# Performance work log

Measured on AMD Instinct MI355X. Metric: run time of the kernel, lower is better.

## Reference

```python
import jax, jax.numpy as jnp
import numpy as np

DIM = 768; HEADS = 12; HD = DIM // HEADS; SCALE = HD ** -0.5
B = 4; T = 8; H = 14; W = 14; N = H * W  # 196 VMAE patches per frame
DOWN = 192   # adapter down dim = dim * 0.25
MLP_H = 3072 # dim * mlp_ratio

def _ln(x, g, b, eps=1e-5):
    m = x.mean(-1, keepdims=True)
    v = ((x - m) ** 2).mean(-1, keepdims=True)
    return (x - m) * jax.lax.rsqrt(v + eps) * g + b

def _lin(x, w, b=None):
    y = x @ w.T
    return y if b is None else y + b

def _gelu(x):
    return jax.nn.gelu(x, approximate=False)  # torch nn.GELU (erf)

def _mha(q, k, v):  # q:[b,h,n,d] k,v:[b,h,m,d]
    a = jax.nn.softmax((q * SCALE) @ jnp.swapaxes(k, -2, -1), axis=-1)
    return a @ v

def _adapter(x, w1, b1, w2, b2, skip):
    y = _lin(_gelu(_lin(x, w1, b1)), w2, b2)
    return x + y if skip else y

def _block(s_x, t_x, p):
    # --- self-attention on temporal (VMAE) tokens, with adapter ---
    xn = _ln(t_x, p['g1'], p['bb1'])
    bias = jnp.concatenate([p['q_bias'], jnp.zeros_like(p['v_bias']), p['v_bias']])
    Bx, Nx, _ = xn.shape
    qkv = _lin(xn, p['qkv_w'], bias).reshape(Bx, Nx, 3, HEADS, HD).transpose(2, 0, 3, 1, 4)
    o = _mha(qkv[0], qkv[1], qkv[2]).transpose(0, 2, 1, 3).reshape(Bx, Nx, DIM)
    o = _lin(o, p['aproj_w'], p['aproj_b'])
    t = t_x + _adapter(o, p['sa_w1'], p['sa_b1'], p['sa_w2'], p['sa_b2'], True)
    # --- S2T cross-attn: temporal queries attend to per-frame CNN spatial tokens ---
    s_pat = s_x.reshape(B * T, H * W, DIM) + p['s2t_pos_cnn']
    tx = t.reshape(B * T, N, DIM) + p['s2t_pos_vmae']
    q = _lin(tx, p['s2t_qw'], p['s2t_qb']).reshape(B * T, N, HEADS, HD).transpose(0, 2, 1, 3)
    kv = _lin(s_pat, p['s2t_kvw'], p['s2t_kvb']).reshape(B * T, H * W, 2, HEADS, HD).transpose(2, 0, 3, 1, 4)
    o = _mha(q, kv[0], kv[1]).transpose(0, 2, 1, 3).reshape(B * T, N, DIM)
    o = _lin(o, p['s2t_pw'], p['s2t_pb']).reshape(B, T * N, DIM)
    t = t + o
    # --- T2S cross-attn: per-location CNN queries attend over time to VMAE tokens ---
    s_pat = s_x.reshape(B, T, H * W, DIM).transpose(0, 2, 1, 3) + p['t2s_pos_cnn']  # b hw t c
    tx = t.reshape(B, T, N, DIM).transpose(0, 2, 1, 3) + p['t2s_pos_vmae']          # b n t d (N==H*W)
    s_pat = s_pat.reshape(B * H * W, T, DIM)
    tx = tx.reshape(B * N, T, DIM)
    q = _lin(s_pat, p['t2s_qw'], p['t2s_qb']).reshape(B * H * W, T, HEADS, HD).transpose(0, 2, 1, 3)
    kv = _lin(tx, p['t2s_kvw'], p['t2s_kvb']).reshape(B * N, T, 2, HEADS, HD).transpose(2, 0, 3, 1, 4)
    o = _mha(q, kv[0], kv[1]).transpose(0, 2, 1, 3).reshape(B * H * W, T, DIM)
    o = _lin(o, p['t2s_pw'], p['t2s_pb'])
    s = s_x + o.reshape(B, H, W, T, DIM).transpose(0, 3, 1, 2, 4).reshape(B * T, H, W, DIM)
    # --- MLP + parallel adapter (scale = 0.5 per Block.__init__) ---
    xn2 = _ln(t, p['g2'], p['bb2'])
    t = t + _lin(_gelu(_lin(xn2, p['fc1_w'], p['fc1_b'])), p['fc2_w'], p['fc2_b']) \
          + 0.5 * _adapter(xn2, p['ma_w1'], p['ma_b1'], p['ma_w2'], p['ma_b2'], False)
    return s, t

PARAM_NAMES = ['g1','bb1','qkv_w','q_bias','v_bias','aproj_w','aproj_b',
               'sa_w1','sa_b1','sa_w2','sa_b2',
               's2t_pos_cnn','s2t_pos_vmae','s2t_qw','s2t_qb','s2t_kvw','s2t_kvb','s2t_pw','s2t_pb',
               't2s_pos_cnn','t2s_pos_vmae','t2s_qw','t2s_qb','t2s_kvw','t2s_kvb','t2s_pw','t2s_pb',
               'g2','bb2','fc1_w','fc1_b','fc2_w','fc2_b','ma_w1','ma_b1','ma_w2','ma_b2']

def setup_inputs():
    key = jax.random.key(0)
    ks = iter(jax.random.split(key, 64))
    def w(shape, s=0.02):
        return jax.random.normal(next(ks), shape, jnp.float32) * s
    d = dict(
        s_x=jax.random.normal(next(ks), (B * T, H, W, DIM), jnp.float32),
        t_x=jax.random.normal(next(ks), (B, T * N, DIM), jnp.float32),
        g1=jnp.ones((DIM,), jnp.float32), bb1=jnp.zeros((DIM,), jnp.float32),
        qkv_w=w((3 * DIM, DIM)), q_bias=jnp.zeros((DIM,), jnp.float32), v_bias=jnp.zeros((DIM,), jnp.float32),
        aproj_w=w((DIM, DIM)), aproj_b=jnp.zeros((DIM,), jnp.float32),
        sa_w1=w((DOWN, DIM)), sa_b1=jnp.zeros((DOWN,), jnp.float32),
        sa_w2=w((DIM, DOWN)), sa_b2=jnp.zeros((DIM,), jnp.float32),
        s2t_pos_cnn=w((H * W, DIM), SCALE), s2t_pos_vmae=w((196, DIM), SCALE),
        s2t_qw=w((DIM, DIM)), s2t_qb=jnp.zeros((DIM,), jnp.float32),
        s2t_kvw=w((2 * DIM, DIM)), s2t_kvb=jnp.zeros((2 * DIM,), jnp.float32),
        s2t_pw=w((DIM, DIM)), s2t_pb=jnp.zeros((DIM,), jnp.float32),
        t2s_pos_cnn=w((T, DIM), SCALE), t2s_pos_vmae=w((T, DIM), SCALE),
        t2s_qw=w((DIM, DIM)), t2s_qb=jnp.zeros((DIM,), jnp.float32),
        t2s_kvw=w((2 * DIM, DIM)), t2s_kvb=jnp.zeros((2 * DIM,), jnp.float32),
        t2s_pw=w((DIM, DIM)), t2s_pb=jnp.zeros((DIM,), jnp.float32),
        g2=jnp.ones((DIM,), jnp.float32), bb2=jnp.zeros((DIM,), jnp.float32),
        fc1_w=w((MLP_H, DIM)), fc1_b=jnp.zeros((MLP_H,), jnp.float32),
        fc2_w=w((DIM, MLP_H)), fc2_b=jnp.zeros((DIM,), jnp.float32),
        ma_w1=w((DOWN, DIM)), ma_b1=jnp.zeros((DOWN,), jnp.float32),
        ma_w2=w((DIM, DOWN)), ma_b2=jnp.zeros((DIM,), jnp.float32),
    )
    return d

def reference(s_x, t_x, g1, bb1, qkv_w, q_bias, v_bias, aproj_w, aproj_b,
              sa_w1, sa_b1, sa_w2, sa_b2,
              s2t_pos_cnn, s2t_pos_vmae, s2t_qw, s2t_qb, s2t_kvw, s2t_kvb, s2t_pw, s2t_pb,
              t2s_pos_cnn, t2s_pos_vmae, t2s_qw, t2s_qb, t2s_kvw, t2s_kvb, t2s_pw, t2s_pb,
              g2, bb2, fc1_w, fc1_b, fc2_w, fc2_b, ma_w1, ma_b1, ma_w2, ma_b2):
    loc = locals()
    p = {k: loc[k] for k in PARAM_NAMES}
    return _block(s_x, t_x, p)
```

## Files before the change

kernel.cpp:

```cpp
#include <hip/hip_runtime.h>
#include <hip/hip_bf16.h>
#include <math.h>


typedef __bf16 bf16_t;
typedef bf16_t bf16x4 __attribute__((ext_vector_type(4)));
typedef bf16_t bf16x8 __attribute__((ext_vector_type(8)));
typedef float  f32x4  __attribute__((ext_vector_type(4)));

typedef const __attribute__((address_space(1))) void* gas_t;
typedef __attribute__((address_space(3))) void* las_t;
__device__ __forceinline__ void async16(const void* g, void* l) {
    __builtin_amdgcn_global_load_lds((gas_t)g, (las_t)l, 16, 0, 0);
}

#define MFMA(a,b,c) __builtin_amdgcn_mfma_f32_16x16x32_bf16((a),(b),(c),0,0,0)
#define EXP2(x) __builtin_amdgcn_exp2f(x)
#define LOG2E 1.4426950408889634f

template<bool GELU>
__global__ __launch_bounds__(256) void gemm128(
    const bf16_t* __restrict__ A, const bf16_t* __restrict__ W,
    const float* __restrict__ bias,
    const float* __restrict__ res1, const float* __restrict__ res2,
    float res2_scale,
    float* __restrict__ Yf, bf16_t* __restrict__ Yb,
    int M, int N, int K)
{
    __shared__ bf16_t As[128*64];
    __shared__ bf16_t Bs[128*64];
    const int tid = threadIdx.x, wave = tid >> 6, lane = tid & 63;
    const int m0 = blockIdx.y * 128, n0 = blockIdx.x * 128;
    const int wm = (wave & 1) * 64, wn = (wave >> 1) * 64;
    const int l15 = lane & 15, lq = lane >> 4;
    const int lrow = lane >> 3, lcol = (lane & 7) * 8;

    f32x4 acc[4][4] = {};

    for (int k0 = 0; k0 < K; k0 += 64) {
#pragma unroll
        for (int c = 0; c < 4; ++c) {
            const int r = wave * 32 + c * 8;
            async16(A + (size_t)(m0 + r + lrow) * K + k0 + lcol, &As[r * 64]);
            async16(W + (size_t)(n0 + r + lrow) * K + k0 + lcol, &Bs[r * 64]);
        }
        __syncthreads();
#pragma unroll
        for (int kk = 0; kk < 64; kk += 32) {
            bf16x8 a[4], b[4];
#pragma unroll
            for (int i = 0; i < 4; ++i)
                a[i] = *(const bf16x8*)&As[(wm + i * 16 + l15) * 64 + kk + lq * 8];
#pragma unroll
            for (int i = 0; i < 4; ++i)
                b[i] = *(const bf16x8*)&Bs[(wn + i * 16 + l15) * 64 + kk + lq * 8];
#pragma unroll
            for (int mi = 0; mi < 4; ++mi)
#pragma unroll
                for (int ni = 0; ni < 4; ++ni)
                    acc[mi][ni] = MFMA(a[mi], b[ni], acc[mi][ni]);
        }
        __syncthreads();
    }

#pragma unroll
    for (int mi = 0; mi < 4; ++mi)
#pragma unroll
    for (int ni = 0; ni < 4; ++ni) {
        const int gn = n0 + wn + ni * 16 + l15;
        const float bv = bias ? bias[gn] : 0.f;
#pragma unroll
        for (int i = 0; i < 4; ++i) {
            const int gm = m0 + wm + mi * 16 + lq * 4 + i;
            float v = acc[mi][ni][i] + bv;
            if (GELU) v = 0.5f * v * (1.0f + erff(v * 0.70710678118654752f));
            const size_t off = (size_t)gm * N + gn;
            if (res1) v += res1[off];
            if (res2) v += res2_scale * res2[off];
            if (Yf) Yf[off] = v;
            if (Yb) Yb[off] = (bf16_t)v;
        }
    }
}

template<bool GELU, int EPI>
__global__ __launch_bounds__(256) void gemm128x64(
    const bf16_t* __restrict__ A, const bf16_t* __restrict__ W,
    const float* __restrict__ bias,
    const float* __restrict__ res1, const float* __restrict__ res2,
    float res2_scale,
    float* __restrict__ Yf, bf16_t* __restrict__ Yb,
    int M, int N, int K,
    const float* __restrict__ ep_a, float* __restrict__ ep_fo,
    bf16_t* __restrict__ ep_bo)
{
    __shared__ bf16_t As[128*64];
    __shared__ bf16_t Bs[64*64];
    const int tid = threadIdx.x, wave = tid >> 6, lane = tid & 63;
    const int m0 = blockIdx.y * 128, n0 = blockIdx.x * 64;
    const int wm = (wave & 1) * 64, wn = (wave >> 1) * 32;
    const int l15 = lane & 15, lq = lane >> 4;
    const int lrow = lane >> 3, lcol = (lane & 7) * 8;

    f32x4 acc[4][2] = {};

    for (int k0 = 0; k0 < K; k0 += 64) {
#pragma unroll
        for (int c = 0; c < 4; ++c) {
            const int r = wave * 32 + c * 8;
            async16(A + (size_t)(m0 + r + lrow) * K + k0 + lcol, &As[r * 64]);
        }
#pragma unroll
        for (int c = 0; c < 2; ++c) {
            const int r = wave * 16 + c * 8;
            async16(W + (size_t)(n0 + r + lrow) * K + k0 + lcol, &Bs[r * 64]);
        }
        __syncthreads();
#pragma unroll
        for (int kk = 0; kk < 64; kk += 32) {
            bf16x8 a[4], b[2];
#pragma unroll
            for (int i = 0; i < 4; ++i)
                a[i] = *(const bf16x8*)&As[(wm + i * 16 + l15) * 64 + kk + lq * 8];
#pragma unroll
            for (int i = 0; i < 2; ++i)
                b[i] = *(const bf16x8*)&Bs[(wn + i * 16 + l15) * 64 + kk + lq * 8];
#pragma unroll
            for (int mi = 0; mi < 4; ++mi)
#pragma unroll
                for (int ni = 0; ni < 2; ++ni)
                    acc[mi][ni] = MFMA(a[mi], b[ni], acc[mi][ni]);
        }
        __syncthreads();
    }

#pragma unroll
    for (int mi = 0; mi < 4; ++mi)
#pragma unroll
    for (int ni = 0; ni < 2; ++ni) {
        const int gn = n0 + wn + ni * 16 + l15;
        const float bv = bias ? bias[gn] : 0.f;
#pragma unroll
        for (int i = 0; i < 4; ++i) {
            const int gm = m0 + wm + mi * 16 + lq * 4 + i;
            float v = acc[mi][ni][i] + bv;
            if (GELU) v = 0.5f * v * (1.0f + erff(v * 0.70710678118654752f));
            const size_t off = (size_t)gm * N + gn;
            if (res1) v += res1[off];
            if (res2) v += res2_scale * res2[off];
            if (Yf) Yf[off] = v;
            if (Yb) Yb[off] = (bf16_t)v;
            if (EPI == 1) {
                const int b_ = gm / 1568, r_ = gm - b_ * 1568;
                const int t_ = r_ / 196,  n_ = r_ - t_ * 196;
                const int dest = ((b_ * 196 + n_) << 3) + t_;
                ep_bo[(size_t)dest * 768 + gn] =
                    (bf16_t)(v + ep_a[t_ * 768 + gn]);
            }
            if (EPI == 2) {
                const int t_ = gm & 7, bn_ = gm >> 3;
                const int n_ = bn_ % 196, b_ = bn_ / 196;
                const int dest = (b_ * 8 + t_) * 196 + n_;
                const size_t doff = (size_t)dest * 768 + gn;
                ep_fo[doff] = ep_a[doff] + v;
            }
        }
    }
}

template<bool GELU, int EPI>
__global__ __launch_bounds__(256) void gemm_bt(
    const float* __restrict__ X, const float* __restrict__ W,
    const float* __restrict__ bias,
    const float* __restrict__ res1, const float* __restrict__ res2,
    float res2_scale,
    float* __restrict__ Y, int M, int N, int K,
    const float* __restrict__ ep_pos, bf16_t* __restrict__ ep_bo)
{
    __shared__ bf16_t As[64][72];
    __shared__ bf16_t Bs[64][72];
    const int tid  = threadIdx.x;
    const int n0   = blockIdx.x * 64;
    const int m0   = blockIdx.y * 64;
    const int wave = tid >> 6, lane = tid & 63;
    const int wm   = (wave & 1) * 32, wn = (wave >> 1) * 32;
    const int l15  = lane & 15, lq = lane >> 4;
    f32x4 acc[2][2] = {};
    const int sr = tid >> 4;
    const int sc4 = (tid & 15) * 4;

    for (int k0 = 0; k0 < K; k0 += 64) {
#pragma unroll
        for (int i = 0; i < 4; ++i) {
            const int row = sr + i * 16;
            const float4 xv = *reinterpret_cast<const float4*>(
                X + (size_t)(m0 + row) * K + k0 + sc4);
            bf16x4 p;
            p[0] = (bf16_t)xv.x; p[1] = (bf16_t)xv.y;
            p[2] = (bf16_t)xv.z; p[3] = (bf16_t)xv.w;
            *reinterpret_cast<bf16x4*>(&As[row][sc4]) = p;
        }
#pragma unroll
        for (int i = 0; i < 4; ++i) {
            const int row = sr + i * 16;
            const float4 wv = *reinterpret_cast<const float4*>(
                W + (size_t)(n0 + row) * K + k0 + sc4);
            bf16x4 p;
            p[0] = (bf16_t)wv.x; p[1] = (bf16_t)wv.y;
            p[2] = (bf16_t)wv.z; p[3] = (bf16_t)wv.w;
            *reinterpret_cast<bf16x4*>(&Bs[row][sc4]) = p;
        }
        __syncthreads();
#pragma unroll
        for (int kk = 0; kk < 64; kk += 32) {
            bf16x8 a0 = *reinterpret_cast<const bf16x8*>(&As[wm +      l15][kk + lq * 8]);
            bf16x8 a1 = *reinterpret_cast<const bf16x8*>(&As[wm + 16 + l15][kk + lq * 8]);
            bf16x8 b0 = *reinterpret_cast<const bf16x8*>(&Bs[wn +      l15][kk + lq * 8]);
            bf16x8 b1 = *reinterpret_cast<const bf16x8*>(&Bs[wn + 16 + l15][kk + lq * 8]);
            acc[0][0] = MFMA(a0, b0, acc[0][0]);
            acc[0][1] = MFMA(a0, b1, acc[0][1]);
            acc[1][0] = MFMA(a1, b0, acc[1][0]);
            acc[1][1] = MFMA(a1, b1, acc[1][1]);
        }
        __syncthreads();
    }

#pragma unroll
    for (int mt = 0; mt < 2; ++mt)
#pragma unroll
    for (int nt = 0; nt < 2; ++nt) {
        const int gn = n0 + wn + nt * 16 + l15;
        const float bv = bias[gn];
#pragma unroll
        for (int i = 0; i < 4; ++i) {
            const int gm = m0 + wm + mt * 16 + lq * 4 + i;
            float v = acc[mt][nt][i] + bv;
            if (GELU) v = 0.5f * v * (1.0f + erff(v * 0.70710678118654752f));
            const size_t off = (size_t)gm * N + gn;
            if (res1) v += res1[off];
            if (res2) v += res2_scale * res2[off];
            Y[off] = v;
            if (EPI == 1) {
                const int n_ = gm % 196;
                ep_bo[off] = (bf16_t)(v + ep_pos[n_ * 768 + gn]);
            }
        }
    }
}

__global__ __launch_bounds__(256) void flash_k(
    const bf16_t* __restrict__ Q, int ldq,
    const bf16_t* __restrict__ Kp, int ldk,
    const bf16_t* __restrict__ Vp, int ldv,
    bf16_t* __restrict__ O, int ldo,
    int nq, int nk, float scale)
{
    __shared__ bf16_t Ks[64 * 68];
    __shared__ bf16_t Vs[64 * 68];
    __shared__ bf16_t Ps[64 * 68];

    const int tid = threadIdx.x, wave = tid >> 6, lane = tid & 63;
    const int q0 = blockIdx.x * 64, hoff = blockIdx.y * 64, g = blockIdx.z;
    const int l15 = lane & 15, lq = lane >> 4;
    const int wm16 = wave * 16;
    const int sr = tid >> 3, sc8 = (tid & 7) * 8;
    const float sl2e = scale * LOG2E;

    bf16x8 bq0, bq1;
    {
        int qr = q0 + wm16 + l15; if (qr > nq - 1) qr = nq - 1;
        const bf16_t* qp = Q + ((size_t)g * nq + qr) * ldq + hoff + lq * 8;
        bq0 = *(const bf16x8*)qp;
        bq1 = *(const bf16x8*)(qp + 32);
    }

    bf16x8 ka, kb, va, vb;
    {
        int r0 = sr;      if (r0 > nk - 1) r0 = nk - 1;
        int r1 = sr + 32; if (r1 > nk - 1) r1 = nk - 1;
        ka = *(const bf16x8*)(Kp + ((size_t)g * nk + r0) * ldk + hoff + sc8);
        kb = *(const bf16x8*)(Kp + ((size_t)g * nk + r1) * ldk + hoff + sc8);
        int key = lane; if (key > nk - 1) key = nk - 1;
        const bf16_t* vp = Vp + ((size_t)g * nk + key) * ldv + hoff + wm16;
        va = *(const bf16x8*)vp;
        vb = *(const bf16x8*)(vp + 8);
    }

    float m_r = -INFINITY, l_r = 0.f;
    f32x4 acc[4] = {};

    for (int kk0 = 0; kk0 < nk; kk0 += 64) {
        __syncthreads();
        *(bf16x8*)&Ks[sr * 68 + sc8] = ka;
        *(bf16x8*)&Ks[(sr + 32) * 68 + sc8] = kb;
#pragma unroll
        for (int j = 0; j < 8; ++j) Vs[(wm16 + j) * 68 + lane] = va[j];
#pragma unroll
        for (int j = 0; j < 8; ++j) Vs[(wm16 + 8 + j) * 68 + lane] = vb[j];
        __syncthreads();

        const int nx = kk0 + 64;
        if (nx < nk) {
            int r0 = nx + sr;      if (r0 > nk - 1) r0 = nk - 1;
            int r1 = nx + sr + 32; if (r1 > nk - 1) r1 = nk - 1;
            ka = *(const bf16x8*)(Kp + ((size_t)g * nk + r0) * ldk + hoff + sc8);
            kb = *(const bf16x8*)(Kp + ((size_t)g * nk + r1) * ldk + hoff + sc8);
            int key = nx + lane; if (key > nk - 1) key = nk - 1;
            const bf16_t* vp = Vp + ((size_t)g * nk + key) * ldv + hoff + wm16;
            va = *(const bf16x8*)vp;
            vb = *(const bf16x8*)(vp + 8);
        }

        f32x4 s[4] = {};
#pragma unroll
        for (int nt = 0; nt < 4; ++nt) {
            bf16x8 ak0 = *(const bf16x8*)&Ks[(nt * 16 + l15) * 68 + lq * 8];
            bf16x8 ak1 = *(const bf16x8*)&Ks[(nt * 16 + l15) * 68 + 32 + lq * 8];
            s[nt] = MFMA(ak0, bq0, s[nt]);
            s[nt] = MFMA(ak1, bq1, s[nt]);
        }

#pragma unroll
        for (int nt = 0; nt < 4; ++nt)
#pragma unroll
        for (int i = 0; i < 4; ++i) {
            const bool valid = (kk0 + nt * 16 + lq * 4 + i) < nk;
            s[nt][i] = valid ? s[nt][i] * sl2e : -INFINITY;
        }

        float t0 = fmaxf(fmaxf(s[0][0], s[0][1]), fmaxf(s[0][2], s[0][3]));
        float t1 = fmaxf(fmaxf(s[1][0], s[1][1]), fmaxf(s[1][2], s[1][3]));
        float t2 = fmaxf(fmaxf(s[2][0], s[2][1]), fmaxf(s[2][2], s[2][3]));
        float t3 = fmaxf(fmaxf(s[3][0], s[3][1]), fmaxf(s[3][2], s[3][3]));
        float t = fmaxf(fmaxf(t0, t1), fmaxf(t2, t3));
        t = fmaxf(t, __shfl_xor(t, 16));
        t = fmaxf(t, __shfl_xor(t, 32));
        const float mnew = fmaxf(m_r, t);
        const float a = EXP2(m_r - mnew);
        float ps = 0.f;
#pragma unroll
        for (int nt = 0; nt < 4; ++nt)
#pragma unroll
        for (int i = 0; i < 4; ++i) {
            const float e = EXP2(s[nt][i] - mnew);
            s[nt][i] = e; ps += e;
        }
        ps += __shfl_xor(ps, 16);
        ps += __shfl_xor(ps, 32);
        l_r = l_r * a + ps;
        m_r = mnew;

        float alq[4];
#pragma unroll
        for (int i = 0; i < 4; ++i) alq[i] = __shfl(a, lq * 4 + i);

#pragma unroll
        for (int nt = 0; nt < 4; ++nt) {
            bf16x4 pk;
            pk[0] = (bf16_t)s[nt][0]; pk[1] = (bf16_t)s[nt][1];
            pk[2] = (bf16_t)s[nt][2]; pk[3] = (bf16_t)s[nt][3];
            *(bf16x4*)&Ps[(wm16 + l15) * 68 + nt * 16 + lq * 4] = pk;
        }

#pragma unroll
        for (int nt = 0; nt < 4; ++nt)
#pragma unroll
        for (int i = 0; i < 4; ++i)
            acc[nt][i] *= alq[i];
#pragma unroll
        for (int kk = 0; kk < 64; kk += 32) {
            bf16x8 ap = *(const bf16x8*)&Ps[(wm16 + l15) * 68 + kk + lq * 8];
#pragma unroll
            for (int nt = 0; nt < 4; ++nt) {
                bf16x8 bv = *(const bf16x8*)&Vs[(nt * 16 + l15) * 68 + kk + lq * 8];
                acc[nt] = MFMA(ap, bv, acc[nt]);
            }
        }
    }

    float linv[4];
#pragma unroll
    for (int i = 0; i < 4; ++i)
        linv[i] = __builtin_amdgcn_rcpf(__shfl(l_r, lq * 4 + i));
#pragma unroll
    for (int nt = 0; nt < 4; ++nt)
#pragma unroll
    for (int i = 0; i < 4; ++i) {
        const int qrow = q0 + wm16 + lq * 4 + i;
        if (qrow < nq)
            O[((size_t)g * nq + qrow) * ldo + hoff + nt * 16 + l15] =
                (bf16_t)(acc[nt][i] * linv[i]);
    }
}

__global__ __launch_bounds__(256) void attn8_k(
    const bf16_t* __restrict__ Q, int ldq,
    const bf16_t* __restrict__ Kp, int ldk,
    const bf16_t* __restrict__ Vp, int ldv,
    bf16_t* __restrict__ O, int ldo,
    float scale)
{
    __shared__ float Ps[4][8][8];
    const int wv = threadIdx.x >> 6, lane = threadIdx.x & 63;
    const int gw  = blockIdx.x * 4 + wv;
    const int seq = gw / 12, h = gw - seq * 12;
    const int hoff = h * 64;
    const int l15 = lane & 15, lq = lane >> 4;
    const size_t rbase = (size_t)seq * 8;
    const float sl2e = scale * LOG2E;

    const int qr = l15 & 7;
    const bf16_t* qp = Q  + (rbase + qr) * ldq + hoff + lq * 8;
    const bf16_t* kp = Kp + (rbase + qr) * ldk + hoff + lq * 8;
    bf16x8 a0 = *(const bf16x8*)qp;
    bf16x8 a1 = *(const bf16x8*)(qp + 32);
    bf16x8 b0 = *(const bf16x8*)kp;
    bf16x8 b1 = *(const bf16x8*)(kp + 32);
    f32x4 z = {};
    f32x4 s = MFMA(a1, b1, MFMA(a0, b0, z));

    const bool cvalid = l15 < 8;
    float p[4];
#pragma unroll
    for (int i = 0; i < 4; ++i) {
        float v = cvalid ? s[i] * sl2e : -INFINITY;
        float m = v;
        m = fmaxf(m, __shfl_xor(m, 1));
        m = fmaxf(m, __shfl_xor(m, 2));
        m = fmaxf(m, __shfl_xor(m, 4));
        m = fmaxf(m, __shfl_xor(m, 8));
        float e = EXP2(v - m);
        float sum = e;
        sum += __shfl_xor(sum, 1);
        sum += __shfl_xor(sum, 2);
        sum += __shfl_xor(sum, 4);
        sum += __shfl_xor(sum, 8);
        p[i] = e * __builtin_amdgcn_rcpf(sum);
    }
    if (lq < 2 && cvalid) {
#pragma unroll
        for (int i = 0; i < 4; ++i)
            Ps[wv][lq * 4 + i][l15] = p[i];
    }
    __syncthreads();

    const int qi = lane >> 3, dg = lane & 7;
    f32x4 p0 = *(const f32x4*)&Ps[wv][qi][0];
    f32x4 p1 = *(const f32x4*)&Ps[wv][qi][4];
    float acc[8] = {};
#pragma unroll
    for (int k = 0; k < 8; ++k) {
        const bf16x8 vvec = *(const bf16x8*)(Vp + (rbase + k) * ldv + hoff + dg * 8);
        const float pk = (k < 4) ? p0[k] : p1[k - 4];
#pragma unroll
        for (int j = 0; j < 8; ++j) acc[j] += pk * (float)vvec[j];
    }
    bf16x8 o;
#pragma unroll
    for (int j = 0; j < 8; ++j) o[j] = (bf16_t)acc[j];
    *(bf16x8*)(O + (rbase + qi) * ldo + hoff + dg * 8) = o;
}

__global__ __launch_bounds__(256) void ln_k(
    const float* __restrict__ x,
    const float* __restrict__ g, const float* __restrict__ bta,
    float* __restrict__ yf, bf16_t* __restrict__ yb)
{
    __shared__ float rA[4], rB[4];
    const int row = blockIdx.x, tid = threadIdx.x;
    const int wv = tid >> 6, lane = tid & 63;
    const size_t base = (size_t)row * 768;
    const float v0 = x[base + tid];
    const float v1 = x[base + tid + 256];
    const float v2 = x[base + tid + 512];
    float s1 = v0 + v1 + v2;
    float s2 = v0 * v0 + v1 * v1 + v2 * v2;
#pragma unroll
    for (int off = 32; off > 0; off >>= 1) {
        s1 += __shfl_xor(s1, off);
        s2 += __shfl_xor(s2, off);
    }
    if (lane == 0) { rA[wv] = s1; rB[wv] = s2; }
    __syncthreads();
    const float ts1 = rA[0] + rA[1] + rA[2] + rA[3];
    const float ts2 = rB[0] + rB[1] + rB[2] + rB[3];
    const float m = ts1 * (1.f / 768.f);
    const float r = rsqrtf(ts2 * (1.f / 768.f) - m * m + 1e-5f);
    const float o0 = (v0 - m) * r * g[tid]       + bta[tid];
    const float o1 = (v1 - m) * r * g[tid + 256] + bta[tid + 256];
    const float o2 = (v2 - m) * r * g[tid + 512] + bta[tid + 512];
    yb[base + tid]       = (bf16_t)o0;
    yb[base + tid + 256] = (bf16_t)o1;
    yb[base + tid + 512] = (bf16_t)o2;
    if (yf) {
        yf[base + tid]       = o0;
        yf[base + tid + 256] = o1;
        yf[base + tid + 512] = o2;
    }
}

__global__ void addpos_k(const float* __restrict__ src, const float* __restrict__ pos,
                         bf16_t* __restrict__ dst, int nrep) {
    const int row = blockIdx.x, tid = threadIdx.x;
    const size_t base = (size_t)row * 768;
    const size_t pbase = (size_t)(row % nrep) * 768;
    for (int k = 0; k < 3; ++k) {
        int c = tid + k * 256;
        dst[base + c] = (bf16_t)(src[base + c] + pos[pbase + c]);
    }
}
__global__ void t2s_prep_q(const float* __restrict__ sx, const float* __restrict__ pos,
                           bf16_t* __restrict__ dst) {
    const int row = blockIdx.x, tid = threadIdx.x;
    const int t = row & 7, bn = row >> 3, n = bn % 196, b = bn / 196;
    const size_t src = (size_t)((b * 8 + t) * 196 + n) * 768;
    const size_t dbase = (size_t)row * 768;
    const size_t pbase = (size_t)t * 768;
    for (int k = 0; k < 3; ++k) {
        int c = tid + k * 256;
        dst[dbase + c] = (bf16_t)(sx[src + c] + pos[pbase + c]);
    }
}
__global__ void build_qkv_bias(const float* __restrict__ qb,
                               const float* __restrict__ vb,
                               float* __restrict__ dst) {
    int i = blockIdx.x * 256 + threadIdx.x;
    if (i < 768) dst[i] = qb[i];
    else if (i < 1536) dst[i] = 0.f;
    else if (i < 2304) dst[i] = vb[i - 1536];
}

struct WPtrs { const float* p[10]; };
__global__ void wcvt(WPtrs s, bf16_t* __restrict__ dst) {
    const int cum[11] = {0, 442368, 589824, 737280, 1032192, 1179648,
                         1327104, 1622016, 1769472, 2359296, 2949120};
    const int gi = blockIdx.x * 256 + threadIdx.x;
    int seg = 0;
#pragma unroll
    for (int i = 1; i < 10; ++i) if (gi >= cum[i]) seg = i;
    const float4 v = ((const float4*)s.p[seg])[gi - cum[seg]];
    bf16x4 o;
    o[0] = (bf16_t)v.x; o[1] = (bf16_t)v.y; o[2] = (bf16_t)v.z; o[3] = (bf16_t)v.w;
    ((bf16x4*)dst)[gi] = o;
}

#define OFF_QKV    0
#define OFF_APROJ  1769472
#define OFF_S2TQ   2359296
#define OFF_S2TKV  2949120
#define OFF_S2TP   4128768
#define OFF_T2SQ   4718592
#define OFF_T2SKV  5308416
#define OFF_T2SP   6488064
#define OFF_FC1    7077888
#define OFF_FC2    9437184
#define W_TOTAL    11796480

extern "C" void kernel_launch(void* const* d_in, const int* in_sizes, int n_in,
                              void* d_out, int out_size, void* d_ws, size_t ws_size,
                              hipStream_t stream)
{
    typedef const float* fp;
    fp s_x     = (fp)d_in[0];
    fp t_x     = (fp)d_in[1];
    fp g1      = (fp)d_in[2];
    fp bb1     = (fp)d_in[3];
    fp qkv_w   = (fp)d_in[4];
    fp q_bias  = (fp)d_in[5];
    fp v_bias  = (fp)d_in[6];
    fp aproj_w = (fp)d_in[7];
    fp aproj_b = (fp)d_in[8];
    fp sa_w1   = (fp)d_in[9];
    fp sa_b1   = (fp)d_in[10];
    fp sa_w2   = (fp)d_in[11];
    fp sa_b2   = (fp)d_in[12];
    fp s2t_pos_cnn  = (fp)d_in[13];
    fp s2t_pos_vmae = (fp)d_in[14];
    fp s2t_qw  = (fp)d_in[15];
    fp s2t_qb  = (fp)d_in[16];
    fp s2t_kvw = (fp)d_in[17];
    fp s2t_kvb = (fp)d_in[18];
    fp s2t_pw  = (fp)d_in[19];
    fp s2t_pb  = (fp)d_in[20];
    fp t2s_pos_cnn  = (fp)d_in[21];
    fp t2s_pos_vmae = (fp)d_in[22];
    fp t2s_qw  = (fp)d_in[23];
    fp t2s_qb  = (fp)d_in[24];
    fp t2s_kvw = (fp)d_in[25];
    fp t2s_kvb = (fp)d_in[26];
    fp t2s_pw  = (fp)d_in[27];
    fp t2s_pb  = (fp)d_in[28];
    fp g2      = (fp)d_in[29];
    fp bb2     = (fp)d_in[30];
    fp fc1_w   = (fp)d_in[31];
    fp fc1_b   = (fp)d_in[32];
    fp fc2_w   = (fp)d_in[33];
    fp fc2_b   = (fp)d_in[34];
    fp ma_w1   = (fp)d_in[35];
    fp ma_b1   = (fp)d_in[36];
    fp ma_w2   = (fp)d_in[37];
    fp ma_b2   = (fp)d_in[38];

    const size_t RD = (size_t)6272 * 768;

    float* ws   = (float*)d_ws;
    float* F    = ws;
    float* G    = F + RD;
    float* CI   = G + RD;
    float* Hb   = CI + RD;
    float* qkvb = Hb + (size_t)6272 * 192;
    bf16_t* BW  = (bf16_t*)(qkvb + 2304);
    bf16_t* Xb  = BW + W_TOTAL;
    bf16_t* Eb  = Xb + RD;
    bf16_t* Fb  = Eb + RD;
    bf16_t* MB  = Fb + RD;
    bf16_t* Xkv = MB + (size_t)6272 * 1536;

    float* out_s = (float*)d_out;
    float* out_t = out_s + RD;

    const dim3 blk(256);

    WPtrs wp;
    wp.p[0] = qkv_w;  wp.p[1] = aproj_w; wp.p[2] = s2t_qw; wp.p[3] = s2t_kvw;
    wp.p[4] = s2t_pw; wp.p[5] = t2s_qw;  wp.p[6] = t2s_kvw; wp.p[7] = t2s_pw;
    wp.p[8] = fc1_w;  wp.p[9] = fc2_w;
    wcvt<<<11520, blk, 0, stream>>>(wp, BW);

    ln_k<<<6272, blk, 0, stream>>>(t_x, g1, bb1, nullptr, Xb);
    build_qkv_bias<<<9, blk, 0, stream>>>(q_bias, v_bias, qkvb);
    gemm128<false><<<dim3(18, 49), blk, 0, stream>>>(
        Xb, BW + OFF_QKV, qkvb, nullptr, nullptr, 0.f, nullptr, MB, 6272, 2304, 768);
    flash_k<<<dim3(25, 12, 4), blk, 0, stream>>>(
        MB, 2304, MB + 768, 2304, MB + 1536, 2304, Eb, 768, 1568, 1568, 0.125f);
    gemm128x64<false, 0><<<dim3(12, 49), blk, 0, stream>>>(
        Eb, BW + OFF_APROJ, aproj_b, nullptr, nullptr, 0.f, F, nullptr, 6272, 768, 768,
        nullptr, nullptr, nullptr);
    gemm_bt<true, 0><<<dim3(3, 98), blk, 0, stream>>>(
        F, sa_w1, sa_b1, nullptr, nullptr, 0.f, Hb, 6272, 192, 768, nullptr, nullptr);
    gemm_bt<false, 1><<<dim3(12, 98), blk, 0, stream>>>(
        Hb, sa_w2, sa_b2, F, t_x, 1.0f, G, 6272, 768, 192, s2t_pos_vmae, Xb);

    gemm128x64<false, 0><<<dim3(12, 49), blk, 0, stream>>>(
        Xb, BW + OFF_S2TQ, s2t_qb, nullptr, nullptr, 0.f, nullptr, Eb, 6272, 768, 768,
        nullptr, nullptr, nullptr);
    addpos_k<<<6272, blk, 0, stream>>>(s_x, s2t_pos_cnn, Xb, 196);
    gemm128<false><<<dim3(12, 49), blk, 0, stream>>>(
        Xb, BW + OFF_S2TKV, s2t_kvb, nullptr, nullptr, 0.f, nullptr, MB, 6272, 1536, 768);
    flash_k<<<dim3(4, 12, 32), blk, 0, stream>>>(
        Eb, 768, MB, 1536, MB + 768, 1536, Fb, 768, 196, 196, 0.125f);
    gemm128x64<false, 1><<<dim3(12, 49), blk, 0, stream>>>(
        Fb, BW + OFF_S2TP, s2t_pb, G, nullptr, 0.f, G, nullptr, 6272, 768, 768,
        t2s_pos_vmae, nullptr, Xkv);

    t2s_prep_q<<<6272, blk, 0, stream>>>(s_x, t2s_pos_cnn, Xb);
    gemm128x64<false, 0><<<dim3(12, 49), blk, 0, stream>>>(
        Xb, BW + OFF_T2SQ, t2s_qb, nullptr, nullptr, 0.f, nullptr, Eb, 6272, 768, 768,
        nullptr, nullptr, nullptr);
    gemm128<false><<<dim3(12, 49), blk, 0, stream>>>(
        Xkv, BW + OFF_T2SKV, t2s_kvb, nullptr, nullptr, 0.f, nullptr, MB, 6272, 1536, 768);
    attn8_k<<<dim3(2352), blk, 0, stream>>>(
        Eb, 768, MB, 1536, MB + 768, 1536, Fb, 768, 0.125f);
    gemm128x64<false, 2><<<dim3(12, 49), blk, 0, stream>>>(
        Fb, BW + OFF_T2SP, t2s_pb, nullptr, nullptr, 0.f, nullptr, nullptr, 6272, 768, 768,
        s_x, out_s, nullptr);

    ln_k<<<6272, blk, 0, stream>>>(G, g2, bb2, CI, Xb);
    gemm128<true><<<dim3(24, 49), blk, 0, stream>>>(
        Xb, BW + OFF_FC1, fc1_b, nullptr, nullptr, 0.f, nullptr, MB, 6272, 3072, 768);
    gemm_bt<true, 0><<<dim3(3, 98), blk, 0, stream>>>(
        CI, ma_w1, ma_b1, nullptr, nullptr, 0.f, Hb, 6272, 192, 768, nullptr, nullptr);
    gemm_bt<false, 0><<<dim3(12, 98), blk, 0, stream>>>(
        Hb, ma_w2, ma_b2, nullptr, nullptr, 0.f, F, 6272, 768, 192, nullptr, nullptr);
    gemm128x64<false, 0><<<dim3(12, 49), blk, 0, stream>>>(
        MB, BW + OFF_FC2, fc2_b, G, F, 0.5f, out_t, nullptr, 6272, 768, 3072,
        nullptr, nullptr, nullptr);
}
```

Before: 929.8 us.

## Write V transposed from QKV GEMM epilogue for vectorized flash V loads

The QKV and S2T KV GEMMs gain an epilogue that also stores the V slice in a per-(batch, head) transposed [dim, seq] layout. The flash attention kernel then loads V rows with 16-byte vector loads and writes LDS with vector stores, replacing per-element scattered transposing writes into LDS. This costs an extra transposed write of V from the GEMM, which is scattered 8-byte stores, plus extra workspace. The T2S KV GEMM and FC1 keep the old path.

```diff
diff --git a/kernel.cpp b/kernel.cpp
--- a/kernel.cpp
+++ b/kernel.cpp
@@ -18,14 +18,15 @@
 #define EXP2(x) __builtin_amdgcn_exp2f(x)
 #define LOG2E 1.4426950408889634f
 
-template<bool GELU>
+template<bool GELU, int EPI>
 __global__ __launch_bounds__(256) void gemm128(
     const bf16_t* __restrict__ A, const bf16_t* __restrict__ W,
     const float* __restrict__ bias,
     const float* __restrict__ res1, const float* __restrict__ res2,
     float res2_scale,
     float* __restrict__ Yf, bf16_t* __restrict__ Yb,
-    int M, int N, int K)
+    int M, int N, int K,
+    bf16_t* __restrict__ ep_vt, int vseq, int vcol0)
 {
     __shared__ bf16_t As[128*64];
     __shared__ bf16_t Bs[128*64];
@@ -69,6 +70,7 @@
     for (int ni = 0; ni < 4; ++ni) {
         const int gn = n0 + wn + ni * 16 + l15;
         const float bv = bias ? bias[gn] : 0.f;
+        float vv[4];
 #pragma unroll
         for (int i = 0; i < 4; ++i) {
             const int gm = m0 + wm + mi * 16 + lq * 4 + i;
@@ -79,6 +81,15 @@
             if (res2) v += res2_scale * res2[off];
             if (Yf) Yf[off] = v;
             if (Yb) Yb[off] = (bf16_t)v;
+            vv[i] = v;
+        }
+        if (EPI == 3 && gn >= vcol0) {
+            const int gm0 = m0 + wm + mi * 16 + lq * 4;
+            const int b_ = gm0 / vseq, key = gm0 - b_ * vseq;
+            bf16x4 pk;
+            pk[0] = (bf16_t)vv[0]; pk[1] = (bf16_t)vv[1];
+            pk[2] = (bf16_t)vv[2]; pk[3] = (bf16_t)vv[3];
+            *(bf16x4*)(ep_vt + ((size_t)(b_ * 768 + gn - vcol0)) * vseq + key) = pk;
         }
     }
 }
@@ -251,7 +262,7 @@
 __global__ __launch_bounds__(256) void flash_k(
     const bf16_t* __restrict__ Q, int ldq,
     const bf16_t* __restrict__ Kp, int ldk,
-    const bf16_t* __restrict__ Vp, int ldv,
+    const bf16_t* __restrict__ Vt,
     bf16_t* __restrict__ O, int ldo,
     int nq, int nk, float scale)
 {
@@ -260,11 +271,13 @@
     __shared__ bf16_t Ps[64 * 68];
 
     const int tid = threadIdx.x, wave = tid >> 6, lane = tid & 63;
-    const int q0 = blockIdx.x * 64, hoff = blockIdx.y * 64, g = blockIdx.z;
+    const int q0 = blockIdx.x * 64, head = blockIdx.y, g = blockIdx.z;
+    const int hoff = head * 64;
     const int l15 = lane & 15, lq = lane >> 4;
     const int wm16 = wave * 16;
     const int sr = tid >> 3, sc8 = (tid & 7) * 8;
     const float sl2e = scale * LOG2E;
+    const bf16_t* vt = Vt + ((size_t)(g * 12 + head) * 64) * nk;
 
     bf16x8 bq0, bq1;
     {
@@ -274,16 +287,27 @@
         bq1 = *(const bf16x8*)(qp + 32);
     }
 
+    auto load_vt = [&](int base, bf16x8& va_, bf16x8& vb_) {
+        if (base + 64 <= nk) {
+            va_ = *(const bf16x8*)(vt + (size_t)sr * nk + base + sc8);
+            vb_ = *(const bf16x8*)(vt + (size_t)(sr + 32) * nk + base + sc8);
+        } else {
+#pragma unroll
+            for (int j = 0; j < 8; ++j) {
+                int c = base + sc8 + j; if (c > nk - 1) c = nk - 1;
+                va_[j] = vt[(size_t)sr * nk + c];
+                vb_[j] = vt[(size_t)(sr + 32) * nk + c];
+            }
+        }
+    };
+
     bf16x8 ka, kb, va, vb;
     {
         int r0 = sr;      if (r0 > nk - 1) r0 = nk - 1;
         int r1 = sr + 32; if (r1 > nk - 1) r1 = nk - 1;
         ka = *(const bf16x8*)(Kp + ((size_t)g * nk + r0) * ldk + hoff + sc8);
         kb = *(const bf16x8*)(Kp + ((size_t)g * nk + r1) * ldk + hoff + sc8);
-        int key = lane; if (key > nk - 1) key = nk - 1;
-        const bf16_t* vp = Vp + ((size_t)g * nk + key) * ldv + hoff + wm16;
-        va = *(const bf16x8*)vp;
-        vb = *(const bf16x8*)(vp + 8);
+        load_vt(0, va, vb);
     }
 
     float m_r = -INFINITY, l_r = 0.f;
@@ -293,10 +317,8 @@
         __syncthreads();
         *(bf16x8*)&Ks[sr * 68 + sc8] = ka;
         *(bf16x8*)&Ks[(sr + 32) * 68 + sc8] = kb;
-#pragma unroll
-        for (int j = 0; j < 8; ++j) Vs[(wm16 + j) * 68 + lane] = va[j];
-#pragma unroll
-        for (int j = 0; j < 8; ++j) Vs[(wm16 + 8 + j) * 68 + lane] = vb[j];
+        *(bf16x8*)&Vs[sr * 68 + sc8] = va;
+        *(bf16x8*)&Vs[(sr + 32) * 68 + sc8] = vb;
         __syncthreads();
 
         const int nx = kk0 + 64;
@@ -305,10 +327,7 @@
             int r1 = nx + sr + 32; if (r1 > nk - 1) r1 = nk - 1;
             ka = *(const bf16x8*)(Kp + ((size_t)g * nk + r0) * ldk + hoff + sc8);
             kb = *(const bf16x8*)(Kp + ((size_t)g * nk + r1) * ldk + hoff + sc8);
-            int key = nx + lane; if (key > nk - 1) key = nk - 1;
-            const bf16_t* vp = Vp + ((size_t)g * nk + key) * ldv + hoff + wm16;
-            va = *(const bf16x8*)vp;
-            vb = *(const bf16x8*)(vp + 8);
+            load_vt(nx, va, vb);
         }
 
         f32x4 s[4] = {};
@@ -615,6 +634,8 @@
     bf16_t* Fb  = Eb + RD;
     bf16_t* MB  = Fb + RD;
     bf16_t* Xkv = MB + (size_t)6272 * 1536;
+    bf16_t* Vt1 = MB + (size_t)6272 * 2304;
+    bf16_t* Vt2 = Xkv;
 
     float* out_s = (float*)d_out;
     float* out_t = out_s + RD;
@@ -629,10 +650,11 @@
 
     ln_k<<<6272, blk, 0, stream>>>(t_x, g1, bb1, nullptr, Xb);
     build_qkv_bias<<<9, blk, 0, stream>>>(q_bias, v_bias, qkvb);
-    gemm128<false><<<dim3(18, 49), blk, 0, stream>>>(
-        Xb, BW + OFF_QKV, qkvb, nullptr, nullptr, 0.f, nullptr, MB, 6272, 2304, 768);
+    gemm128<false, 3><<<dim3(18, 49), blk, 0, stream>>>(
+        Xb, BW + OFF_QKV, qkvb, nullptr, nullptr, 0.f, nullptr, MB, 6272, 2304, 768,
+        Vt1, 1568, 1536);
     flash_k<<<dim3(25, 12, 4), blk, 0, stream>>>(
-        MB, 2304, MB + 768, 2304, MB + 1536, 2304, Eb, 768, 1568, 1568, 0.125f);
+        MB, 2304, MB + 768, 2304, Vt1, Eb, 768, 1568, 1568, 0.125f);
     gemm128x64<false, 0><<<dim3(12, 49), blk, 0, stream>>>(
         Eb, BW + OFF_APROJ, aproj_b, nullptr, nullptr, 0.f, F, nullptr, 6272, 768, 768,
         nullptr, nullptr, nullptr);
@@ -645,10 +667,11 @@
         Xb, BW + OFF_S2TQ, s2t_qb, nullptr, nullptr, 0.f, nullptr, Eb, 6272, 768, 768,
         nullptr, nullptr, nullptr);
     addpos_k<<<6272, blk, 0, stream>>>(s_x, s2t_pos_cnn, Xb, 196);
-    gemm128<false><<<dim3(12, 49), blk, 0, stream>>>(
-        Xb, BW + OFF_S2TKV, s2t_kvb, nullptr, nullptr, 0.f, nullptr, MB, 6272, 1536, 768);
+    gemm128<false, 3><<<dim3(12, 49), blk, 0, stream>>>(
+        Xb, BW + OFF_S2TKV, s2t_kvb, nullptr, nullptr, 0.f, nullptr, MB, 6272, 1536, 768,
+        Vt2, 196, 768);
     flash_k<<<dim3(4, 12, 32), blk, 0, stream>>>(
-        Eb, 768, MB, 1536, MB + 768, 1536, Fb, 768, 196, 196, 0.125f);
+        Eb, 768, MB, 1536, Vt2, Fb, 768, 196, 196, 0.125f);
     gemm128x64<false, 1><<<dim3(12, 49), blk, 0, stream>>>(
         Fb, BW + OFF_S2TP, s2t_pb, G, nullptr, 0.f, G, nullptr, 6272, 768, 768,
         t2s_pos_vmae, nullptr, Xkv);
@@ -657,8 +680,9 @@
     gemm128x64<false, 0><<<dim3(12, 49), blk, 0, stream>>>(
         Xb, BW + OFF_T2SQ, t2s_qb, nullptr, nullptr, 0.f, nullptr, Eb, 6272, 768, 768,
         nullptr, nullptr, nullptr);
-    gemm128<false><<<dim3(12, 49), blk, 0, stream>>>(
-        Xkv, BW + OFF_T2SKV, t2s_kvb, nullptr, nullptr, 0.f, nullptr, MB, 6272, 1536, 768);
+    gemm128<false, 0><<<dim3(12, 49), blk, 0, stream>>>(
+        Xkv, BW + OFF_T2SKV, t2s_kvb, nullptr, nullptr, 0.f, nullptr, MB, 6272, 1536, 768,
+        nullptr, 0, 0);
     attn8_k<<<dim3(2352), blk, 0, stream>>>(
         Eb, 768, MB, 1536, MB + 768, 1536, Fb, 768, 0.125f);
     gemm128x64<false, 2><<<dim3(12, 49), blk, 0, stream>>>(
@@ -666,8 +690,9 @@
         s_x, out_s, nullptr);
 
     ln_k<<<6272, blk, 0, stream>>>(G, g2, bb2, CI, Xb);
-    gemm128<true><<<dim3(24, 49), blk, 0, stream>>>(
-        Xb, BW + OFF_FC1, fc1_b, nullptr, nullptr, 0.f, nullptr, MB, 6272, 3072, 768);
+    gemm128<true, 0><<<dim3(24, 49), blk, 0, stream>>>(
+        Xb, BW + OFF_FC1, fc1_b, nullptr, nullptr, 0.f, nullptr, MB, 6272, 3072, 768,
+        nullptr, 0, 0);
     gemm_bt<true, 0><<<dim3(3, 98), blk, 0, stream>>>(
         CI, ma_w1, ma_b1, nullptr, nullptr, 0.f, Hb, 6272, 192, 768, nullptr, nullptr);
     gemm_bt<false, 0><<<dim3(12, 98), blk, 0, stream>>>(
```

Result: slower. 1.044 ms (+12.3%).
